# Optimization experiments

Measured on AMD Instinct MI355X. Metric: run time of the kernel, lower is better.

The kernel has to match this reference:

```python
import jax, jax.numpy as jnp
import numpy as np

HIDDEN = 64


def setup_inputs() -> dict:
    key = jax.random.key(0)
    k1, k2 = jax.random.split(key)
    B, T = 16384, 64
    total = HIDDEN * 5 + 1 + HIDDEN * HIDDEN  # 4417
    coefficients = jax.random.normal(k1, (B, total), dtype=jnp.float32) * 0.1
    last_n_inputs = jax.random.normal(k2, (B, T), dtype=jnp.float32)
    return {"coefficients": coefficients, "last_n_inputs": last_n_inputs}


def _split_coeffs(coefficients, h):
    B = coefficients.shape[0]
    idx = 0
    w_ih = coefficients[:, idx:idx + h]                      # (B, h)  == view(B,h,1) squeezed
    idx += h
    w_hh = coefficients[:, idx:idx + h * h].reshape(B, h, h)  # (B, h, h)
    idx += h * h
    b_ih = coefficients[:, idx:idx + h]
    idx += h
    b_hh = coefficients[:, idx:idx + h]
    idx += h
    fc_w = coefficients[:, idx:idx + h]                      # (B, h)
    idx += h
    fc_b = coefficients[:, idx:idx + 1]                      # (B, 1)
    idx += 1
    h0 = coefficients[:, idx:idx + h]                        # (B, h)
    return w_ih, w_hh, b_ih, b_hh, fc_w, fc_b, h0


def reference(coefficients, last_n_inputs):
    h = HIDDEN
    w_ih, w_hh, b_ih, b_hh, fc_w, fc_b, h0 = _split_coeffs(coefficients, h)
    bias = b_ih + b_hh  # fuse the two bias adds

    def step(hid, x_t):
        # x_t: (B,) scalar input per sample; w_ih: (B,h)
        # torch: bmm(hidden, w_hh^T) -> new[b,k] = sum_j hid[b,j] * w_hh[b,k,j]
        new = jnp.tanh(x_t[:, None] * w_ih + bias
                       + jnp.einsum('bj,bkj->bk', hid, w_hh))
        return new, None

    xs = last_n_inputs.T  # (T, B) scan over time
    hid, _ = jax.lax.scan(step, h0, xs)

    # fc: bmm(hid (B,1,h), fc_w^T (B,h,1)) + fc_b -> (B,1)
    pred = jnp.sum(hid * fc_w, axis=-1, keepdims=True) + fc_b
    return pred
```

## Files before the change

### kernel.cpp

```cpp
#include <hip/hip_runtime.h>
#include <math.h>

#define HIDDEN 64
#define TOTAL  4417
#define TSTEPS 64


__global__ __launch_bounds__(64, 4)
void rnn_fused_kernel(const float* __restrict__ coeff,
                      const float* __restrict__ xin,
                      float* __restrict__ out)
{
    const int b    = blockIdx.x;
    const int lane = threadIdx.x;

    const float* __restrict__ c = coeff + (size_t)b * TOTAL;

    __shared__ __align__(16) float hsh[HIDDEN];

    const float wih  = c[lane];
    const float bias = c[4160 + lane] + c[4224 + lane];
    const float fcw  = c[4288 + lane];
    const float fcb  = c[4352];
    const float h0   = c[4353 + lane];
    const float xv   = xin[(size_t)b * TSTEPS + lane];

    float W[HIDDEN];
    const float* __restrict__ wrow = c + 64 + lane * HIDDEN;
    #pragma unroll
    for (int j = 0; j < HIDDEN; ++j) W[j] = wrow[j];

    hsh[lane] = h0;
    __syncthreads();

    float hn = h0;

    #pragma unroll 1
    for (int t = 0; t < TSTEPS; ++t) {
        const float xt  = __shfl(xv, t, 64);
        float acc = fmaf(xt, wih, bias);

        #pragma unroll
        for (int j4 = 0; j4 < HIDDEN / 4; ++j4) {
            const float4 hv = *reinterpret_cast<const float4*>(&hsh[j4 * 4]);
            acc = fmaf(hv.x, W[4 * j4 + 0], acc);
            acc = fmaf(hv.y, W[4 * j4 + 1], acc);
            acc = fmaf(hv.z, W[4 * j4 + 2], acc);
            acc = fmaf(hv.w, W[4 * j4 + 3], acc);
        }

        const float e = __expf(acc + acc);
        hn = 1.0f - 2.0f * __builtin_amdgcn_rcpf(e + 1.0f);

        __syncthreads();
        hsh[lane] = hn;
        __syncthreads();
    }

    float p = hn * fcw;
    #pragma unroll
    for (int off = 32; off > 0; off >>= 1)
        p += __shfl_xor(p, off, 64);

    if (lane == 0) out[b] = p + fcb;
}

extern "C" void kernel_launch(void* const* d_in, const int* in_sizes, int n_in,
                              void* d_out, int out_size, void* d_ws, size_t ws_size,
                              hipStream_t stream)
{
    const float* coeff = (const float*)d_in[0];
    const float* xin   = (const float*)d_in[1];
    float* out         = (float*)d_out;

    const int B = in_sizes[0] / TOTAL;

    rnn_fused_kernel<<<B, HIDDEN, 0, stream>>>(coeff, xin, out);
}
```

Baseline: 173.0 us.

## Split hidden-state matvec across two wavefronts per sample with LDS partial sums

New measurement: 226.5 us. 30.9% more time.

```diff
diff --git a/kernel.cpp b/kernel.cpp
--- a/kernel.cpp
+++ b/kernel.cpp
@@ -6,17 +6,22 @@
 #define TSTEPS 64
 
 
-__global__ __launch_bounds__(64, 4)
+typedef float f4 __attribute__((ext_vector_type(4)));
+
+__global__ __launch_bounds__(128)
 void rnn_fused_kernel(const float* __restrict__ coeff,
                       const float* __restrict__ xin,
                       float* __restrict__ out)
 {
+    const int tid  = threadIdx.x;
+    const int lane = tid & 63;
+    const int w    = tid >> 6;
     const int b    = blockIdx.x;
-    const int lane = threadIdx.x;
 
     const float* __restrict__ c = coeff + (size_t)b * TOTAL;
 
     __shared__ __align__(16) float hsh[HIDDEN];
+    __shared__ float psh[2][HIDDEN];
 
     const float wih  = c[lane];
     const float bias = c[4160 + lane] + c[4224 + lane];
@@ -25,44 +30,52 @@
     const float h0   = c[4353 + lane];
     const float xv   = xin[(size_t)b * TSTEPS + lane];
 
-    float W[HIDDEN];
-    const float* __restrict__ wrow = c + 64 + lane * HIDDEN;
+    float W[32];
+    const float* __restrict__ wrow = c + HIDDEN + (size_t)lane * HIDDEN + 32 * w;
     #pragma unroll
-    for (int j = 0; j < HIDDEN; ++j) W[j] = wrow[j];
+    for (int j = 0; j < 32; ++j) W[j] = wrow[j];
+    #pragma unroll
+    for (int j = 0; j < 32; ++j) asm volatile("" : "+v"(W[j]));
 
-    hsh[lane] = h0;
+    if (w == 0) hsh[lane] = h0;
     __syncthreads();
+
+    const f4* hp = (const f4*)(hsh + 32 * w);
 
     float hn = h0;
 
     #pragma unroll 1
     for (int t = 0; t < TSTEPS; ++t) {
-        const float xt  = __shfl(xv, t, 64);
-        float acc = fmaf(xt, wih, bias);
+        float a0 = 0.0f, a1 = 0.0f, a2 = 0.0f, a3 = 0.0f;
+        #pragma unroll
+        for (int q = 0; q < 8; ++q) {
+            const f4 hv = hp[q];
+            a0 = fmaf(hv.x, W[4 * q + 0], a0);
+            a1 = fmaf(hv.y, W[4 * q + 1], a1);
+            a2 = fmaf(hv.z, W[4 * q + 2], a2);
+            a3 = fmaf(hv.w, W[4 * q + 3], a3);
+        }
+        psh[w][lane] = (a0 + a1) + (a2 + a3);
 
-        #pragma unroll
-        for (int j4 = 0; j4 < HIDDEN / 4; ++j4) {
-            const float4 hv = *reinterpret_cast<const float4*>(&hsh[j4 * 4]);
-            acc = fmaf(hv.x, W[4 * j4 + 0], acc);
-            acc = fmaf(hv.y, W[4 * j4 + 1], acc);
-            acc = fmaf(hv.z, W[4 * j4 + 2], acc);
-            acc = fmaf(hv.w, W[4 * j4 + 3], acc);
-        }
+        __syncthreads();
 
+        const float xt  = __int_as_float(
+            __builtin_amdgcn_readlane(__float_as_int(xv), t));
+        const float acc = fmaf(xt, wih, bias) + psh[0][lane] + psh[1][lane];
         const float e = __expf(acc + acc);
         hn = 1.0f - 2.0f * __builtin_amdgcn_rcpf(e + 1.0f);
+        hsh[lane] = hn;
 
-        __syncthreads();
-        hsh[lane] = hn;
         __syncthreads();
     }
 
-    float p = hn * fcw;
-    #pragma unroll
-    for (int off = 32; off > 0; off >>= 1)
-        p += __shfl_xor(p, off, 64);
-
-    if (lane == 0) out[b] = p + fcb;
+    if (w == 0) {
+        float p = hn * fcw;
+        #pragma unroll
+        for (int off = 32; off > 0; off >>= 1)
+            p += __shfl_xor(p, off, 64);
+        if (lane == 0) out[b] = p + fcb;
+    }
 }
 
 extern "C" void kernel_launch(void* const* d_in, const int* in_sizes, int n_in,
@@ -75,5 +88,5 @@
 
     const int B = in_sizes[0] / TOTAL;
 
-    rnn_fused_kernel<<<B, HIDDEN, 0, stream>>>(coeff, xin, out);
+    rnn_fused_kernel<<<B, 128, 0, stream>>>(coeff, xin, out);
 }
```

## Rewrite recurrent loop in inline asm with DPP broadcast of hidden state

Applied to the files above, without the earlier changes.

Result: faster. 165.5 us (-4.3%).

```diff
diff --git a/kernel.cpp b/kernel.cpp
--- a/kernel.cpp
+++ b/kernel.cpp
@@ -6,7 +6,15 @@
 #define TSTEPS 64
 
 
-__global__ __launch_bounds__(64, 4)
+#define WL(r, o)   "global_load_dword v" #r ", %[wr], off offset:" #o "\n\t"
+#define DPP4(i, wa, wb, wc, wd) \
+    "v_fmac_f32_dpp v120, v88, v" #wa " row_newbcast:" #i " row_mask:0xf bank_mask:0xf\n\t" \
+    "v_fmac_f32_dpp v121, v89, v" #wb " row_newbcast:" #i " row_mask:0xf bank_mask:0xf\n\t" \
+    "v_fmac_f32_dpp v122, v90, v" #wc " row_newbcast:" #i " row_mask:0xf bank_mask:0xf\n\t" \
+    "v_fmac_f32_dpp v123, v91, v" #wd " row_newbcast:" #i " row_mask:0xf bank_mask:0xf\n\t"
+
+__global__
+__attribute__((amdgpu_flat_work_group_size(64, 64)))
 void rnn_fused_kernel(const float* __restrict__ coeff,
                       const float* __restrict__ xin,
                       float* __restrict__ out)
@@ -16,7 +24,7 @@
 
     const float* __restrict__ c = coeff + (size_t)b * TOTAL;
 
-    __shared__ __align__(16) float hsh[HIDDEN];
+    __shared__ __align__(16) float lds[128];
 
     const float wih  = c[lane];
     const float bias = c[4160 + lane] + c[4224 + lane];
@@ -25,37 +33,87 @@
     const float h0   = c[4353 + lane];
     const float xv   = xin[(size_t)b * TSTEPS + lane];
 
-    float W[HIDDEN];
-    const float* __restrict__ wrow = c + 64 + lane * HIDDEN;
-    #pragma unroll
-    for (int j = 0; j < HIDDEN; ++j) W[j] = wrow[j];
+    const float* wrow = c + HIDDEN + (size_t)lane * HIDDEN;
 
-    hsh[lane] = h0;
-    __syncthreads();
+    const unsigned ha  = (unsigned)(unsigned long long)(const void*)lds;
+    const unsigned hqa = ha + 16u * (unsigned)(lane & 15);
+    const unsigned hw  = ha + 4u  * (unsigned)lane;
 
-    float hn = h0;
+    lds[lane]      = h0;
+    lds[64 + lane] = xv;
 
-    #pragma unroll 1
-    for (int t = 0; t < TSTEPS; ++t) {
-        const float xt  = __shfl(xv, t, 64);
-        float acc = fmaf(xt, wih, bias);
-
-        #pragma unroll
-        for (int j4 = 0; j4 < HIDDEN / 4; ++j4) {
-            const float4 hv = *reinterpret_cast<const float4*>(&hsh[j4 * 4]);
-            acc = fmaf(hv.x, W[4 * j4 + 0], acc);
-            acc = fmaf(hv.y, W[4 * j4 + 1], acc);
-            acc = fmaf(hv.z, W[4 * j4 + 2], acc);
-            acc = fmaf(hv.w, W[4 * j4 + 3], acc);
-        }
-
-        const float e = __expf(acc + acc);
-        hn = 1.0f - 2.0f * __builtin_amdgcn_rcpf(e + 1.0f);
-
-        __syncthreads();
-        hsh[lane] = hn;
-        __syncthreads();
-    }
+    float hn;
+    asm volatile(
+        WL(24,0)  WL(25,4)  WL(26,8)  WL(27,12)  WL(28,16)  WL(29,20)  WL(30,24)  WL(31,28)
+        WL(32,32) WL(33,36) WL(34,40) WL(35,44)  WL(36,48)  WL(37,52)  WL(38,56)  WL(39,60)
+        WL(40,64) WL(41,68) WL(42,72) WL(43,76)  WL(44,80)  WL(45,84)  WL(46,88)  WL(47,92)
+        WL(48,96) WL(49,100) WL(50,104) WL(51,108) WL(52,112) WL(53,116) WL(54,120) WL(55,124)
+        WL(56,128) WL(57,132) WL(58,136) WL(59,140) WL(60,144) WL(61,148) WL(62,152) WL(63,156)
+        WL(64,160) WL(65,164) WL(66,168) WL(67,172) WL(68,176) WL(69,180) WL(70,184) WL(71,188)
+        WL(72,192) WL(73,196) WL(74,200) WL(75,204) WL(76,208) WL(77,212) WL(78,216) WL(79,220)
+        WL(80,224) WL(81,228) WL(82,232) WL(83,236) WL(84,240) WL(85,244) WL(86,248) WL(87,252)
+        "s_mov_b32 s20, 0\n\t"
+        "v_add_u32 v127, 0x100, %[ha]\n\t"
+        "s_waitcnt vmcnt(0)\n\t"
+        "s_waitcnt lgkmcnt(0)\n"
+        "9:\n\t"
+        "ds_read_b32 v126, v127\n\t"
+        "ds_read_b128 v[88:91], %[hqa]\n\t"
+        "v_add_u32 v127, 4, v127\n\t"
+        "s_waitcnt lgkmcnt(0)\n\t"
+        "v_fma_f32 v120, v126, %[wih], %[bias]\n\t"
+        "v_mov_b32 v121, 0\n\t"
+        "v_mov_b32 v122, 0\n\t"
+        "v_mov_b32 v123, 0\n\t"
+        DPP4(0,  24, 25, 26, 27)
+        DPP4(1,  28, 29, 30, 31)
+        DPP4(2,  32, 33, 34, 35)
+        DPP4(3,  36, 37, 38, 39)
+        DPP4(4,  40, 41, 42, 43)
+        DPP4(5,  44, 45, 46, 47)
+        DPP4(6,  48, 49, 50, 51)
+        DPP4(7,  52, 53, 54, 55)
+        DPP4(8,  56, 57, 58, 59)
+        DPP4(9,  60, 61, 62, 63)
+        DPP4(10, 64, 65, 66, 67)
+        DPP4(11, 68, 69, 70, 71)
+        DPP4(12, 72, 73, 74, 75)
+        DPP4(13, 76, 77, 78, 79)
+        DPP4(14, 80, 81, 82, 83)
+        DPP4(15, 84, 85, 86, 87)
+        "v_add_f32 v120, v120, v121\n\t"
+        "v_add_f32 v122, v122, v123\n\t"
+        "v_add_f32 v120, v120, v122\n\t"
+        "v_mul_f32 v125, 0x4038aa3b, v120\n\t"
+        "v_exp_f32 v125, v125\n\t"
+        "s_nop 1\n\t"
+        "v_add_f32 v125, 1.0, v125\n\t"
+        "v_rcp_f32 v125, v125\n\t"
+        "s_nop 1\n\t"
+        "v_fma_f32 v124, -2.0, v125, 1.0\n\t"
+        "ds_write_b32 %[hw], v124\n\t"
+        "s_add_u32 s20, s20, 1\n\t"
+        "s_cmp_lt_u32 s20, 64\n\t"
+        "s_cbranch_scc1 9b\n\t"
+        "s_waitcnt lgkmcnt(0)\n\t"
+        "v_mov_b32 %[hn], v124\n\t"
+        : [hn] "=v"(hn)
+        : [wr] "v"(wrow), [ha] "v"(ha), [hqa] "v"(hqa), [hw] "v"(hw),
+          [wih] "v"(wih), [bias] "v"(bias)
+        : "memory", "scc", "s20",
+          "v24","v25","v26","v27","v28","v29","v30","v31",
+          "v32","v33","v34","v35","v36","v37","v38","v39",
+          "v40","v41","v42","v43","v44","v45","v46","v47",
+          "v48","v49","v50","v51","v52","v53","v54","v55",
+          "v56","v57","v58","v59","v60","v61","v62","v63",
+          "v64","v65","v66","v67","v68","v69","v70","v71",
+          "v72","v73","v74","v75","v76","v77","v78","v79",
+          "v80","v81","v82","v83","v84","v85","v86","v87",
+          "v88","v89","v90","v91","v92","v93","v94","v95",
+          "v96","v97","v98","v99","v100","v101","v102","v103",
+          "v104","v105","v106","v107","v108","v109","v110","v111",
+          "v112","v113","v114","v115","v116","v117","v118","v119",
+          "v120","v121","v122","v123","v124","v125","v126","v127");
 
     float p = hn * fcw;
     #pragma unroll
```
